# Performance work log

Measured on AMD Instinct MI355X. Metric: run time of the kernel, lower is better.

The kernel has to match this reference:

```python
import jax, jax.numpy as jnp
import numpy as np

B, S, D = 2, 2048, 1024
H = 16
HD = D // H  # 64

def setup_inputs() -> dict:
    key = jax.random.key(0)
    ks = jax.random.split(key, 6)
    s = 1.0 / np.sqrt(D)
    return {
        "x": jax.random.normal(ks[0], (B, S, D), dtype=jnp.float32),
        "Wq": jax.random.normal(ks[1], (D, D), dtype=jnp.float32) * s,
        "Wk": jax.random.normal(ks[2], (D, D), dtype=jnp.float32) * s,
        "Wv": jax.random.normal(ks[3], (D, D), dtype=jnp.float32) * s,
        "Wo": jax.random.normal(ks[4], (D, D), dtype=jnp.float32) * s,
        "bo": jax.random.normal(ks[5], (D,), dtype=jnp.float32) * 0.01,
    }

def reference(x, Wq, Wk, Wv, Wo, bo):
    b, n, _ = x.shape
    # qkv projections (nn.Linear: x @ W^T, no bias for qkv)
    q = (x @ Wq.T).reshape(b, n, H, HD).transpose(0, 2, 1, 3)  # [B,H,S,hd]
    k = (x @ Wk.T).reshape(b, n, H, HD).transpose(0, 2, 1, 3)
    v = (x @ Wv.T).reshape(b, n, H, HD).transpose(0, 2, 1, 3)
    scores = jnp.einsum('bhqd,bhkd->bhqk', q, k)  # [B,H,S,S]
    causal = jnp.triu(jnp.ones((n, n), dtype=bool), k=1)
    scores = jnp.where(causal, -jnp.inf, scores)
    attn = jax.nn.softmax(scores / np.sqrt(HD), axis=-1)
    ctx = jnp.einsum('bhqk,bhkd->bhqd', attn, v)  # [B,H,S,hd]
    ctx = ctx.transpose(0, 2, 1, 3).reshape(b, n, D)
    return ctx @ Wo.T + bo
```

## Files before the change

### kernel.cpp

```cpp
#include <hip/hip_runtime.h>
#include <hip/hip_bf16.h>

typedef __hip_bfloat16 bf16;
typedef short v8s __attribute__((ext_vector_type(8)));
typedef float v4f __attribute__((ext_vector_type(4)));

#define S_ 2048
#define D_ 1024
#define H_ 16
#define HD_ 64

#define EXP2F(x) __builtin_amdgcn_exp2f(x)
#define NEG_BIG (-1.0e30f)
#define C2 0.1803368801111244f

#define GLDS16(g, l) __builtin_amdgcn_global_load_lds(                        \
    (const __attribute__((address_space(1))) unsigned int*)(g),               \
    (__attribute__((address_space(3))) unsigned int*)(l), 16, 0, 0)

static __device__ __forceinline__ unsigned short bf16_bits(bf16 h) {
    union { bf16 h; unsigned short u; } c; c.h = h; return c.u;
}

static __device__ __forceinline__ v8s pack_bf16x8(const float4 a, const float4 b) {
    union { v8s v; unsigned short u[8]; } r;
    r.u[0] = bf16_bits(__float2bfloat16(a.x));
    r.u[1] = bf16_bits(__float2bfloat16(a.y));
    r.u[2] = bf16_bits(__float2bfloat16(a.z));
    r.u[3] = bf16_bits(__float2bfloat16(a.w));
    r.u[4] = bf16_bits(__float2bfloat16(b.x));
    r.u[5] = bf16_bits(__float2bfloat16(b.y));
    r.u[6] = bf16_bits(__float2bfloat16(b.z));
    r.u[7] = bf16_bits(__float2bfloat16(b.w));
    return r.v;
}

__global__ __launch_bounds__(256)
void cvt_bf16(const float* __restrict__ x,  const float* __restrict__ wq,
              const float* __restrict__ wk, const float* __restrict__ wv,
              const float* __restrict__ wo,
              bf16* __restrict__ xb,  bf16* __restrict__ wqb,
              bf16* __restrict__ wkb, bf16* __restrict__ wvb,
              bf16* __restrict__ wob)
{
    const int seg = blockIdx.y;
    const float* src; bf16* dst; int n;
    switch (seg) {
        case 0: src = x;  dst = xb;  n = 4096 * 1024; break;
        case 1: src = wq; dst = wqb; n = 1024 * 1024; break;
        case 2: src = wk; dst = wkb; n = 1024 * 1024; break;
        case 3: src = wv; dst = wvb; n = 1024 * 1024; break;
        default:src = wo; dst = wob; n = 1024 * 1024; break;
    }
    const int idx = (blockIdx.x * 256 + threadIdx.x) * 8;
    if (idx >= n) return;
    *(v8s*)&dst[idx] = pack_bf16x8(*(const float4*)&src[idx],
                                   *(const float4*)&src[idx + 4]);
}

__global__ __launch_bounds__(256)
void gemm_qkv_f(const bf16* __restrict__ xb, const bf16* __restrict__ wqb,
                const bf16* __restrict__ wkb, const bf16* __restrict__ wvb,
                bf16* __restrict__ qd, bf16* __restrict__ kd, bf16* __restrict__ vtd)
{
    const int mode = blockIdx.z;
    const bf16* __restrict__ W = (mode == 0) ? wqb : (mode == 1) ? wkb : wvb;
    const int m0 = blockIdx.x * 128;
    const int n0 = blockIdx.y * 128;
    __shared__ bf16 As[128 * 32];
    __shared__ bf16 Bs[128 * 32];
    const int t    = threadIdx.x;
    const int lane = t & 63, w = t >> 6;
    const int wr = w >> 1, wc = w & 1;
    const int l15 = lane & 15, quad = lane >> 4;
    const int r16 = lane >> 2, c8 = (lane & 3) * 8;
    v4f acc[4][4] = {};

    const bf16* ga = &xb[(m0 + w*16 + r16) * 1024 + c8];
    const bf16* gb = &W [(n0 + w*16 + r16) * 1024 + c8];
    bf16* la0 = &As[w * 16 * 32];
    bf16* la1 = &As[(64 + w * 16) * 32];
    bf16* lb0 = &Bs[w * 16 * 32];
    bf16* lb1 = &Bs[(64 + w * 16) * 32];

    for (int k0 = 0; k0 < 1024; k0 += 32) {
        __syncthreads();
        GLDS16(ga + k0,             la0);
        GLDS16(ga + k0 + 64 * 1024, la1);
        GLDS16(gb + k0,             lb0);
        GLDS16(gb + k0 + 64 * 1024, lb1);
        __syncthreads();
        v8s a[4], b[4];
#pragma unroll
        for (int mt = 0; mt < 4; mt++) a[mt] = *(const v8s*)&As[(wr*64 + mt*16 + l15)*32 + quad*8];
#pragma unroll
        for (int nt = 0; nt < 4; nt++) b[nt] = *(const v8s*)&Bs[(wc*64 + nt*16 + l15)*32 + quad*8];
#pragma unroll
        for (int mt = 0; mt < 4; mt++)
#pragma unroll
            for (int nt = 0; nt < 4; nt++)
                acc[mt][nt] = __builtin_amdgcn_mfma_f32_16x16x32_bf16(a[mt], b[nt], acc[mt][nt], 0, 0, 0);
    }

    const float qscale = (mode == 0) ? C2 : 1.0f;
#pragma unroll
    for (int mt = 0; mt < 4; mt++) {
        const int mb = m0 + wr*64 + mt*16 + quad*4;
        const int b_ = mb >> 11, s = mb & 2047;
#pragma unroll
        for (int nt = 0; nt < 4; nt++) {
            const int n = n0 + wc*64 + nt*16 + l15;
            const int h = n >> 6, d = n & 63;
            if (mode == 2) {
                unsigned int lo = (unsigned int)bf16_bits(__float2bfloat16(acc[mt][nt][0]))
                                | ((unsigned int)bf16_bits(__float2bfloat16(acc[mt][nt][1])) << 16);
                unsigned int hi = (unsigned int)bf16_bits(__float2bfloat16(acc[mt][nt][2]))
                                | ((unsigned int)bf16_bits(__float2bfloat16(acc[mt][nt][3])) << 16);
                uint2 pv; pv.x = lo; pv.y = hi;
                *(uint2*)&vtd[((b_*H_ + h)*HD_ + d)*S_ + s] = pv;
            } else {
                bf16* __restrict__ dst = (mode == 0) ? qd : kd;
#pragma unroll
                for (int r = 0; r < 4; r++)
                    dst[((b_*H_ + h)*S_ + (s + r))*HD_ + d] = __float2bfloat16(acc[mt][nt][r] * qscale);
            }
        }
    }
}

__global__ __launch_bounds__(256)
void gemm_out_f(const bf16* __restrict__ ctx, const bf16* __restrict__ wob,
                const float* __restrict__ bo, float* __restrict__ out)
{
    const int m0 = blockIdx.x * 128;
    const int n0 = blockIdx.y * 128;
    __shared__ bf16 As[128 * 32];
    __shared__ bf16 Bs[128 * 32];
    const int t    = threadIdx.x;
    const int lane = t & 63, w = t >> 6;
    const int wr = w >> 1, wc = w & 1;
    const int l15 = lane & 15, quad = lane >> 4;
    const int r16 = lane >> 2, c8 = (lane & 3) * 8;
    v4f acc[4][4] = {};

    const bf16* ga = &ctx[(m0 + w*16 + r16) * 1024 + c8];
    const bf16* gb = &wob[(n0 + w*16 + r16) * 1024 + c8];
    bf16* la0 = &As[w * 16 * 32];
    bf16* la1 = &As[(64 + w * 16) * 32];
    bf16* lb0 = &Bs[w * 16 * 32];
    bf16* lb1 = &Bs[(64 + w * 16) * 32];

    for (int k0 = 0; k0 < 1024; k0 += 32) {
        __syncthreads();
        GLDS16(ga + k0,             la0);
        GLDS16(ga + k0 + 64 * 1024, la1);
        GLDS16(gb + k0,             lb0);
        GLDS16(gb + k0 + 64 * 1024, lb1);
        __syncthreads();
        v8s a[4], b[4];
#pragma unroll
        for (int mt = 0; mt < 4; mt++) a[mt] = *(const v8s*)&As[(wr*64 + mt*16 + l15)*32 + quad*8];
#pragma unroll
        for (int nt = 0; nt < 4; nt++) b[nt] = *(const v8s*)&Bs[(wc*64 + nt*16 + l15)*32 + quad*8];
#pragma unroll
        for (int mt = 0; mt < 4; mt++)
#pragma unroll
            for (int nt = 0; nt < 4; nt++)
                acc[mt][nt] = __builtin_amdgcn_mfma_f32_16x16x32_bf16(a[mt], b[nt], acc[mt][nt], 0, 0, 0);
    }

#pragma unroll
    for (int mt = 0; mt < 4; mt++) {
        const int mb = m0 + wr*64 + mt*16 + quad*4;
#pragma unroll
        for (int nt = 0; nt < 4; nt++) {
            const int n = n0 + wc*64 + nt*16 + l15;
            const float bias = bo[n];
#pragma unroll
            for (int r = 0; r < 4; r++)
                out[(mb + r)*1024 + n] = acc[mt][nt][r] + bias;
        }
    }
}

__global__ __launch_bounds__(256)
void gemm_qkv(const float* __restrict__ x, const float* __restrict__ Wq,
              const float* __restrict__ Wk, const float* __restrict__ Wv,
              bf16* __restrict__ qd, bf16* __restrict__ kd, bf16* __restrict__ vtd)
{
    const int mode = blockIdx.z;
    const float* __restrict__ W = (mode == 0) ? Wq : (mode == 1) ? Wk : Wv;
    const int m0 = blockIdx.x * 128;
    const int n0 = blockIdx.y * 128;
    __shared__ bf16 As[128 * 40];
    __shared__ bf16 Bs[128 * 40];
    const int t    = threadIdx.x;
    const int lane = t & 63, w = t >> 6;
    const int wr = w >> 1, wc = w & 1;
    const int l15 = lane & 15, quad = lane >> 4;
    const int srow = t >> 2, scol = (t & 3) * 8;
    v4f acc[4][4] = {};

    for (int k0 = 0; k0 < 1024; k0 += 32) {
        __syncthreads();
        {
            const float* pa = &x[(m0 + srow) * 1024 + k0 + scol];
            *(v8s*)&As[srow*40 + scol] = pack_bf16x8(*(const float4*)pa, *(const float4*)(pa + 4));
            const float* pa2 = pa + 64 * 1024;
            *(v8s*)&As[(srow+64)*40 + scol] = pack_bf16x8(*(const float4*)pa2, *(const float4*)(pa2 + 4));
            const float* pb = &W[(n0 + srow) * 1024 + k0 + scol];
            *(v8s*)&Bs[srow*40 + scol] = pack_bf16x8(*(const float4*)pb, *(const float4*)(pb + 4));
            const float* pb2 = pb + 64 * 1024;
            *(v8s*)&Bs[(srow+64)*40 + scol] = pack_bf16x8(*(const float4*)pb2, *(const float4*)(pb2 + 4));
        }
        __syncthreads();
        v8s a[4], b[4];
#pragma unroll
        for (int mt = 0; mt < 4; mt++) a[mt] = *(const v8s*)&As[(wr*64 + mt*16 + l15)*40 + quad*8];
#pragma unroll
        for (int nt = 0; nt < 4; nt++) b[nt] = *(const v8s*)&Bs[(wc*64 + nt*16 + l15)*40 + quad*8];
#pragma unroll
        for (int mt = 0; mt < 4; mt++)
#pragma unroll
            for (int nt = 0; nt < 4; nt++)
                acc[mt][nt] = __builtin_amdgcn_mfma_f32_16x16x32_bf16(a[mt], b[nt], acc[mt][nt], 0, 0, 0);
    }

    const float qscale = (mode == 0) ? C2 : 1.0f;
#pragma unroll
    for (int mt = 0; mt < 4; mt++) {
        const int mb = m0 + wr*64 + mt*16 + quad*4;
        const int b_ = mb >> 11, s = mb & 2047;
#pragma unroll
        for (int nt = 0; nt < 4; nt++) {
            const int n = n0 + wc*64 + nt*16 + l15;
            const int h = n >> 6, d = n & 63;
            if (mode == 2) {
                unsigned int lo = (unsigned int)bf16_bits(__float2bfloat16(acc[mt][nt][0]))
                                | ((unsigned int)bf16_bits(__float2bfloat16(acc[mt][nt][1])) << 16);
                unsigned int hi = (unsigned int)bf16_bits(__float2bfloat16(acc[mt][nt][2]))
                                | ((unsigned int)bf16_bits(__float2bfloat16(acc[mt][nt][3])) << 16);
                uint2 pv; pv.x = lo; pv.y = hi;
                *(uint2*)&vtd[((b_*H_ + h)*HD_ + d)*S_ + s] = pv;
            } else {
                bf16* __restrict__ dst = (mode == 0) ? qd : kd;
#pragma unroll
                for (int r = 0; r < 4; r++)
                    dst[((b_*H_ + h)*S_ + (s + r))*HD_ + d] = __float2bfloat16(acc[mt][nt][r] * qscale);
            }
        }
    }
}

__global__ __launch_bounds__(256)
void gemm_out(const bf16* __restrict__ ctx, const float* __restrict__ Wo,
              const float* __restrict__ bo, float* __restrict__ out)
{
    const int m0 = blockIdx.x * 128;
    const int n0 = blockIdx.y * 128;
    __shared__ bf16 As[128 * 40];
    __shared__ bf16 Bs[128 * 40];
    const int t    = threadIdx.x;
    const int lane = t & 63, w = t >> 6;
    const int wr = w >> 1, wc = w & 1;
    const int l15 = lane & 15, quad = lane >> 4;
    const int srow = t >> 2, scol = (t & 3) * 8;
    v4f acc[4][4] = {};

    for (int k0 = 0; k0 < 1024; k0 += 32) {
        __syncthreads();
        {
            *(v8s*)&As[srow*40 + scol]      = *(const v8s*)&ctx[(m0+srow)*1024 + k0 + scol];
            *(v8s*)&As[(srow+64)*40 + scol] = *(const v8s*)&ctx[(m0+srow+64)*1024 + k0 + scol];
            const float* pb = &Wo[(n0 + srow) * 1024 + k0 + scol];
            *(v8s*)&Bs[srow*40 + scol] = pack_bf16x8(*(const float4*)pb, *(const float4*)(pb + 4));
            const float* pb2 = pb + 64 * 1024;
            *(v8s*)&Bs[(srow+64)*40 + scol] = pack_bf16x8(*(const float4*)pb2, *(const float4*)(pb2 + 4));
        }
        __syncthreads();
        v8s a[4], b[4];
#pragma unroll
        for (int mt = 0; mt < 4; mt++) a[mt] = *(const v8s*)&As[(wr*64 + mt*16 + l15)*40 + quad*8];
#pragma unroll
        for (int nt = 0; nt < 4; nt++) b[nt] = *(const v8s*)&Bs[(wc*64 + nt*16 + l15)*40 + quad*8];
#pragma unroll
        for (int mt = 0; mt < 4; mt++)
#pragma unroll
            for (int nt = 0; nt < 4; nt++)
                acc[mt][nt] = __builtin_amdgcn_mfma_f32_16x16x32_bf16(a[mt], b[nt], acc[mt][nt], 0, 0, 0);
    }

#pragma unroll
    for (int mt = 0; mt < 4; mt++) {
        const int mb = m0 + wr*64 + mt*16 + quad*4;
#pragma unroll
        for (int nt = 0; nt < 4; nt++) {
            const int n = n0 + wc*64 + nt*16 + l15;
            const float bias = bo[n];
#pragma unroll
            for (int r = 0; r < 4; r++)
                out[(mb + r)*1024 + n] = acc[mt][nt][r] + bias;
        }
    }
}

__global__ __launch_bounds__(512)
void flash_attn(const bf16* __restrict__ qd, const bf16* __restrict__ kd,
                const bf16* __restrict__ vtd, bf16* __restrict__ ctx)
{
    const int bh = blockIdx.x;
    const int p  = blockIdx.y;
    const int t = threadIdx.x;
    const int lane = t & 63, w = t >> 6;
    const int l15 = lane & 15, quad = lane >> 4;
    const int side = w >> 2, wl = w & 3;
    const int q0 = (side ? (15 - p) : p) * 128;
    const int nT = 32 - 2 * p;

    __shared__ bf16 Vs[2][64 * 72];
    __shared__ bf16 Pl[8][16 * 72];

    const int mrow0 = q0 + wl * 16;
    const int mrow1 = q0 + 64 + wl * 16;

    v8s qf[2][2];
#pragma unroll
    for (int mt = 0; mt < 2; mt++) {
        const bf16* qb_ = qd + (bh*S_ + (mt ? mrow1 : mrow0) + l15) * HD_;
        qf[mt][0] = *(const v8s*)(qb_ + quad*8);
        qf[mt][1] = *(const v8s*)(qb_ + 32 + quad*8);
    }

    v4f o[2][4] = {};
    float ps[2][4] = {};

    const int rowlo = t >> 3, col8 = (t & 7) * 8;
    const bf16* vp = vtd + (bh*HD_ + rowlo)*S_ + col8;
    v8s pv = *(const v8s*)vp;

    const bf16* kbase = kd + (size_t)bh * S_ * HD_;
    v8s kf[4][2];
#pragma unroll
    for (int kt = 0; kt < 4; kt++) {
        const bf16* kp_ = kbase + (kt*16 + l15)*HD_ + quad*8;
        kf[kt][0] = *(const v8s*)kp_;
        kf[kt][1] = *(const v8s*)(kp_ + 32);
    }

    for (int it = 0; it < nT; ++it) {
        const int c0 = it * 64;
        bf16* Vb = &Vs[it & 1][0];
        *(v8s*)&Vb[rowlo*72 + col8] = pv;
        __syncthreads();
        vp += 64;
        pv = *(const v8s*)vp;

        const bool act  = (c0      <= mrow1 + 15);
        const bool nact = (c0 + 64 <= mrow1 + 15);
        v8s nkf[4][2];
        if (nact) {
#pragma unroll
            for (int kt = 0; kt < 4; kt++) {
                const bf16* kp_ = kbase + (c0 + 64 + kt*16 + l15)*HD_ + quad*8;
                nkf[kt][0] = *(const v8s*)kp_;
                nkf[kt][1] = *(const v8s*)(kp_ + 32);
            }
        }

        if (act) {
            v8s vf[4][2];
#pragma unroll
            for (int dt = 0; dt < 4; dt++) {
                vf[dt][0] = *(const v8s*)&Vb[(dt*16 + l15)*72 + quad*8];
                vf[dt][1] = *(const v8s*)&Vb[(dt*16 + l15)*72 + 32 + quad*8];
            }

#pragma unroll
            for (int mt = 0; mt < 2; mt++) {
                const int mr = mt ? mrow1 : mrow0;
                if (c0 > mr + 15) continue;
                v4f sc[4] = {};
#pragma unroll
                for (int kt = 0; kt < 4; kt++) {
                    sc[kt] = __builtin_amdgcn_mfma_f32_16x16x32_bf16(qf[mt][0], kf[kt][0], sc[kt], 0, 0, 0);
                    sc[kt] = __builtin_amdgcn_mfma_f32_16x16x32_bf16(qf[mt][1], kf[kt][1], sc[kt], 0, 0, 0);
                }
                const bool full = (c0 + 63 <= mr);
#pragma unroll
                for (int r = 0; r < 4; r++) {
                    const int qg = mr + quad*4 + r;
#pragma unroll
                    for (int kt = 0; kt < 4; kt++) {
                        float s = sc[kt][r];
                        if (!full) {
                            const int kg = c0 + kt*16 + l15;
                            s = (kg <= qg) ? s : NEG_BIG;
                        }
                        const float pp = EXP2F(s);
                        sc[kt][r] = pp;
                        ps[mt][r] += pp;
                    }
                }
                bf16* pw = &Pl[w][0];
#pragma unroll
                for (int kt = 0; kt < 4; kt++)
#pragma unroll
                    for (int r = 0; r < 4; r++)
                        pw[(quad*4 + r)*72 + kt*16 + l15] = __float2bfloat16(sc[kt][r]);
                v8s pf0 = *(const v8s*)&pw[l15*72 + quad*8];
                v8s pf1 = *(const v8s*)&pw[l15*72 + 32 + quad*8];
#pragma unroll
                for (int dt = 0; dt < 4; dt++) {
                    o[mt][dt] = __builtin_amdgcn_mfma_f32_16x16x32_bf16(pf0, vf[dt][0], o[mt][dt], 0, 0, 0);
                    o[mt][dt] = __builtin_amdgcn_mfma_f32_16x16x32_bf16(pf1, vf[dt][1], o[mt][dt], 0, 0, 0);
                }
            }
        }
        if (nact) {
#pragma unroll
            for (int kt = 0; kt < 4; kt++) { kf[kt][0] = nkf[kt][0]; kf[kt][1] = nkf[kt][1]; }
        }
    }

    const int b_ = bh >> 4, h = bh & 15;
#pragma unroll
    for (int mt = 0; mt < 2; mt++) {
        const int mr = mt ? mrow1 : mrow0;
#pragma unroll
        for (int r = 0; r < 4; r++) {
            float l = ps[mt][r];
#pragma unroll
            for (int off = 1; off < 16; off <<= 1) l += __shfl_xor(l, off);
            const float linv = 1.0f / l;
            const int qg = mr + quad*4 + r;
#pragma unroll
            for (int dt = 0; dt < 4; dt++)
                ctx[(b_*S_ + qg)*D_ + h*HD_ + dt*16 + l15] = __float2bfloat16(o[mt][dt][r] * linv);
        }
    }
}

extern "C" void kernel_launch(void* const* d_in, const int* in_sizes, int n_in,
                              void* d_out, int out_size, void* d_ws, size_t ws_size,
                              hipStream_t stream) {
    const float* x  = (const float*)d_in[0];
    const float* Wq = (const float*)d_in[1];
    const float* Wk = (const float*)d_in[2];
    const float* Wv = (const float*)d_in[3];
    const float* Wo = (const float*)d_in[4];
    const float* bo = (const float*)d_in[5];
    float* out = (float*)d_out;

    const size_t SEG = (size_t)2 * H_ * S_ * HD_;
    bf16* qd  = (bf16*)d_ws;
    bf16* kd  = qd  + SEG;
    bf16* vtd = kd  + SEG;
    bf16* xc  = vtd + SEG;
    bf16* wqb = xc + SEG;
    bf16* wkb = wqb + 1024 * 1024;
    bf16* wvb = wkb + 1024 * 1024;
    bf16* wob = wvb + 1024 * 1024;

    const size_t need_fast = (4 * SEG + 4 * 1024 * 1024) * sizeof(bf16);

    if (ws_size >= need_fast) {
        cvt_bf16<<<dim3(2048, 5), 256, 0, stream>>>(x, Wq, Wk, Wv, Wo,
                                                    xc, wqb, wkb, wvb, wob);
        gemm_qkv_f<<<dim3(32, 8, 3), 256, 0, stream>>>(xc, wqb, wkb, wvb, qd, kd, vtd);
        flash_attn<<<dim3(32, 8), 512, 0, stream>>>(qd, kd, vtd, xc);
        gemm_out_f<<<dim3(32, 8), 256, 0, stream>>>(xc, wob, bo, out);
    } else {
        gemm_qkv<<<dim3(32, 8, 3), 256, 0, stream>>>(x, Wq, Wk, Wv, qd, kd, vtd);
        flash_attn<<<dim3(32, 8), 512, 0, stream>>>(qd, kd, vtd, xc);
        gemm_out<<<dim3(32, 8), 256, 0, stream>>>(xc, Wo, bo, out);
    }
}
```

Measured before the change: 208.4 us.

## Replace QKV GEMM with 256x256 tile, 8-wave, ping-pong pipelined kernel

Swaps the 128x128, single-stage QKV projection GEMM for a 256x256 tile kernel with 8 waves, double-buffered 64-wide K chunks staged through direct global-to-LDS loads. It interleaves LDS fragment loads, async staging of the next chunk, and MFMA quadrants, separated by barriers, with raised wave priority around the MFMA bursts. The goal is to hide global load latency and raise data reuse per tile. In exchange it uses much more LDS and registers, and launches only 192 blocks, which may underfill the GPU.

```diff
diff --git a/kernel.cpp b/kernel.cpp
--- a/kernel.cpp
+++ b/kernel.cpp
@@ -58,71 +58,116 @@
                                    *(const float4*)&src[idx + 4]);
 }
 
-__global__ __launch_bounds__(256)
-void gemm_qkv_f(const bf16* __restrict__ xb, const bf16* __restrict__ wqb,
-                const bf16* __restrict__ wkb, const bf16* __restrict__ wvb,
-                bf16* __restrict__ qd, bf16* __restrict__ kd, bf16* __restrict__ vtd)
+static __device__ __forceinline__ void stage_half(bf16* ldsbase, const bf16* gbase,
+                                                  int w, int l) {
+    const int r = l >> 3, c = (l & 7) * 8;
+    GLDS16(gbase + (size_t)((2 * w + 0) * 8 + r) * 1024 + c, ldsbase + (2 * w + 0) * 512);
+    GLDS16(gbase + (size_t)((2 * w + 1) * 8 + r) * 1024 + c, ldsbase + (2 * w + 1) * 512);
+}
+
+#define MF16(a, b, c) __builtin_amdgcn_mfma_f32_16x16x32_bf16(a, b, c, 0, 0, 0)
+
+#define LDA(buf, mf0) { _Pragma("unroll") for (int m_ = 0; m_ < 4; ++m_) {     \
+    af[m_][0] = *(const v8s*)&AsS[(buf)*16384 + abase + ((mf0) + m_)*1024];    \
+    af[m_][1] = *(const v8s*)&AsS[(buf)*16384 + abase + ((mf0) + m_)*1024 + 32]; } }
+#define LDB0(buf) { _Pragma("unroll") for (int n_ = 0; n_ < 2; ++n_) {         \
+    b0f[n_][0] = *(const v8s*)&BsS[(buf)*16384 + bbase + n_*1024];             \
+    b0f[n_][1] = *(const v8s*)&BsS[(buf)*16384 + bbase + n_*1024 + 32]; } }
+#define LDB1(buf) { _Pragma("unroll") for (int n_ = 0; n_ < 2; ++n_) {         \
+    b1f[n_][0] = *(const v8s*)&BsS[(buf)*16384 + bbase + (2 + n_)*1024];       \
+    b1f[n_][1] = *(const v8s*)&BsS[(buf)*16384 + bbase + (2 + n_)*1024 + 32]; } }
+#define MMQ(MH, NH, AF, BF) { _Pragma("unroll") for (int m_ = 0; m_ < 4; ++m_) \
+    _Pragma("unroll") for (int n_ = 0; n_ < 2; ++n_) {                         \
+      acc[(MH)*4 + m_][(NH)*2 + n_] =                                          \
+        MF16(AF[m_][0], BF[n_][0], acc[(MH)*4 + m_][(NH)*2 + n_]);             \
+      acc[(MH)*4 + m_][(NH)*2 + n_] =                                          \
+        MF16(AF[m_][1], BF[n_][1], acc[(MH)*4 + m_][(NH)*2 + n_]); } }
+#define BAR() __builtin_amdgcn_s_barrier()
+#define VMC2() asm volatile("s_waitcnt vmcnt(2)" ::: "memory")
+#define PRIO1() __builtin_amdgcn_s_setprio(1)
+#define PRIO0() __builtin_amdgcn_s_setprio(0)
+
+__global__ __launch_bounds__(512, 2)
+void gemm_qkv_8p(const bf16* __restrict__ xb, const bf16* __restrict__ wqb,
+                 const bf16* __restrict__ wkb, const bf16* __restrict__ wvb,
+                 bf16* __restrict__ qd, bf16* __restrict__ kd, bf16* __restrict__ vtd)
 {
+    __shared__ bf16 AsS[2 * 16384];
+    __shared__ bf16 BsS[2 * 16384];
     const int mode = blockIdx.z;
     const bf16* __restrict__ W = (mode == 0) ? wqb : (mode == 1) ? wkb : wvb;
-    const int m0 = blockIdx.x * 128;
-    const int n0 = blockIdx.y * 128;
-    __shared__ bf16 As[128 * 32];
-    __shared__ bf16 Bs[128 * 32];
-    const int t    = threadIdx.x;
+    const int m0 = blockIdx.x * 256;
+    const int n0 = blockIdx.y * 256;
+    const int t = threadIdx.x;
     const int lane = t & 63, w = t >> 6;
-    const int wr = w >> 1, wc = w & 1;
+    const int wr = w >> 2, wc = w & 3;
     const int l15 = lane & 15, quad = lane >> 4;
-    const int r16 = lane >> 2, c8 = (lane & 3) * 8;
-    v4f acc[4][4] = {};
-
-    const bf16* ga = &xb[(m0 + w*16 + r16) * 1024 + c8];
-    const bf16* gb = &W [(n0 + w*16 + r16) * 1024 + c8];
-    bf16* la0 = &As[w * 16 * 32];
-    bf16* la1 = &As[(64 + w * 16) * 32];
-    bf16* lb0 = &Bs[w * 16 * 32];
-    bf16* lb1 = &Bs[(64 + w * 16) * 32];
-
-    for (int k0 = 0; k0 < 1024; k0 += 32) {
-        __syncthreads();
-        GLDS16(ga + k0,             la0);
-        GLDS16(ga + k0 + 64 * 1024, la1);
-        GLDS16(gb + k0,             lb0);
-        GLDS16(gb + k0 + 64 * 1024, lb1);
-        __syncthreads();
-        v8s a[4], b[4];
-#pragma unroll
-        for (int mt = 0; mt < 4; mt++) a[mt] = *(const v8s*)&As[(wr*64 + mt*16 + l15)*32 + quad*8];
-#pragma unroll
-        for (int nt = 0; nt < 4; nt++) b[nt] = *(const v8s*)&Bs[(wc*64 + nt*16 + l15)*32 + quad*8];
-#pragma unroll
-        for (int mt = 0; mt < 4; mt++)
-#pragma unroll
-            for (int nt = 0; nt < 4; nt++)
-                acc[mt][nt] = __builtin_amdgcn_mfma_f32_16x16x32_bf16(a[mt], b[nt], acc[mt][nt], 0, 0, 0);
+    const int abase = wr * 8192 + l15 * 64 + quad * 8;
+    const int bbase = (wc >> 1) * 8192 + (wc & 1) * 4096 + l15 * 64 + quad * 8;
+    const bf16* Aap = xb + (size_t)m0 * 1024;
+    const bf16* Bbp = W + (size_t)n0 * 1024;
+
+    v4f acc[8][4] = {};
+    v8s af[4][2], b0f[2][2], b1f[2][2];
+
+    stage_half(AsS,          Aap,          w, lane);
+    stage_half(AsS + 8192,   Aap + 131072, w, lane);
+    stage_half(BsS,          Bbp,          w, lane);
+    stage_half(BsS + 8192,   Bbp + 131072, w, lane);
+    stage_half(AsS + 16384,  Aap + 64,     w, lane);
+    VMC2();
+    BAR();
+
+    for (int i = 0; i < 8; ++i) {
+        const int kc = i * 128;
+        LDA(0, 0); LDB0(0);
+        stage_half(AsS + 16384 + 8192, Aap + 131072 + kc + 64, w, lane);
+        BAR(); PRIO1(); MMQ(0, 0, af, b0f); PRIO0(); BAR();
+        LDB1(0);
+        stage_half(BsS + 16384, Bbp + kc + 64, w, lane);
+        BAR(); PRIO1(); MMQ(0, 1, af, b1f); PRIO0(); BAR();
+        LDA(0, 4);
+        stage_half(BsS + 16384 + 8192, Bbp + 131072 + kc + 64, w, lane);
+        BAR(); PRIO1(); MMQ(1, 1, af, b1f); PRIO0(); BAR();
+        stage_half(AsS, Aap + kc + 128, w, lane);
+        VMC2();
+        BAR(); PRIO1(); MMQ(1, 0, af, b0f); PRIO0(); BAR();
+        LDA(1, 0); LDB0(1);
+        stage_half(AsS + 8192, Aap + 131072 + kc + 128, w, lane);
+        BAR(); PRIO1(); MMQ(0, 0, af, b0f); PRIO0(); BAR();
+        LDB1(1);
+        stage_half(BsS, Bbp + kc + 128, w, lane);
+        BAR(); PRIO1(); MMQ(0, 1, af, b1f); PRIO0(); BAR();
+        LDA(1, 4);
+        stage_half(BsS + 8192, Bbp + 131072 + kc + 128, w, lane);
+        BAR(); PRIO1(); MMQ(1, 1, af, b1f); PRIO0(); BAR();
+        stage_half(AsS + 16384, Aap + kc + 192, w, lane);
+        VMC2();
+        BAR(); PRIO1(); MMQ(1, 0, af, b0f); PRIO0(); BAR();
     }
 
     const float qscale = (mode == 0) ? C2 : 1.0f;
 #pragma unroll
-    for (int mt = 0; mt < 4; mt++) {
-        const int mb = m0 + wr*64 + mt*16 + quad*4;
+    for (int mf = 0; mf < 8; ++mf) {
+        const int mb = m0 + wr * 128 + mf * 16 + quad * 4;
         const int b_ = mb >> 11, s = mb & 2047;
 #pragma unroll
-        for (int nt = 0; nt < 4; nt++) {
-            const int n = n0 + wc*64 + nt*16 + l15;
+        for (int nf = 0; nf < 4; ++nf) {
+            const int n = n0 + wc * 64 + nf * 16 + l15;
             const int h = n >> 6, d = n & 63;
             if (mode == 2) {
-                unsigned int lo = (unsigned int)bf16_bits(__float2bfloat16(acc[mt][nt][0]))
-                                | ((unsigned int)bf16_bits(__float2bfloat16(acc[mt][nt][1])) << 16);
-                unsigned int hi = (unsigned int)bf16_bits(__float2bfloat16(acc[mt][nt][2]))
-                                | ((unsigned int)bf16_bits(__float2bfloat16(acc[mt][nt][3])) << 16);
+                unsigned int lo = (unsigned int)bf16_bits(__float2bfloat16(acc[mf][nf][0]))
+                                | ((unsigned int)bf16_bits(__float2bfloat16(acc[mf][nf][1])) << 16);
+                unsigned int hi = (unsigned int)bf16_bits(__float2bfloat16(acc[mf][nf][2]))
+                                | ((unsigned int)bf16_bits(__float2bfloat16(acc[mf][nf][3])) << 16);
                 uint2 pv; pv.x = lo; pv.y = hi;
-                *(uint2*)&vtd[((b_*H_ + h)*HD_ + d)*S_ + s] = pv;
+                *(uint2*)&vtd[((b_ * H_ + h) * HD_ + d) * S_ + s] = pv;
             } else {
                 bf16* __restrict__ dst = (mode == 0) ? qd : kd;
 #pragma unroll
-                for (int r = 0; r < 4; r++)
-                    dst[((b_*H_ + h)*S_ + (s + r))*HD_ + d] = __float2bfloat16(acc[mt][nt][r] * qscale);
+                for (int r = 0; r < 4; ++r)
+                    dst[((b_ * H_ + h) * S_ + (s + r)) * HD_ + d] =
+                        __float2bfloat16(acc[mf][nf][r] * qscale);
             }
         }
     }
@@ -466,7 +511,7 @@
     if (ws_size >= need_fast) {
         cvt_bf16<<<dim3(2048, 5), 256, 0, stream>>>(x, Wq, Wk, Wv, Wo,
                                                     xc, wqb, wkb, wvb, wob);
-        gemm_qkv_f<<<dim3(32, 8, 3), 256, 0, stream>>>(xc, wqb, wkb, wvb, qd, kd, vtd);
+        gemm_qkv_8p<<<dim3(16, 4, 3), 512, 0, stream>>>(xc, wqb, wkb, wvb, qd, kd, vtd);
         flash_attn<<<dim3(32, 8), 512, 0, stream>>>(qd, kd, vtd, xc);
         gemm_out_f<<<dim3(32, 8), 256, 0, stream>>>(xc, wob, bo, out);
     } else {
```

Result: no change. 211.6 us (+1.5%).
